# Performance work log

Hardware: AMD Instinct MI355X
Metric: run time of the kernel (lower is better)

Reference implementation:

```python
import jax, jax.numpy as jnp
import numpy as np

SHIFT = 1  # module's random shift_direction, fixed to +1 for determinism
B, C, H, W_SP = 1024, 512, 7, 7


def setup_inputs() -> dict:
    key = jax.random.key(0)
    k1, k2 = jax.random.split(key)
    x = jax.random.normal(k1, (B, C, H, W_SP), dtype=jnp.float32)
    W = jax.random.normal(k2, (256, 3, 3, 512), dtype=jnp.float32)
    return {"x": x, "W": W}


def _forward(x, W):
    # unfold along H with kernel (3,1), padding (1,0):
    # patches[b,c,kh,h,w] = x_padded[b,c,h+kh,w]
    xp = jnp.pad(x, ((0, 0), (0, 0), (1, 1), (0, 0)))
    t2 = jnp.stack([xp[:, :, k:k + H, :] for k in range(3)], axis=2)  # (B,512,3,7,7)
    # split channels 512 -> (2,256), move group dim next to H
    t2 = t2.reshape(B, 2, 256, 3, H, W_SP)
    t2 = t2.transpose(0, 2, 3, 4, 1, 5)          # (B,256,3,7,2,7)
    t2 = t2.reshape(B, 256, 3, 14, W_SP)         # interleave (h,group) -> 14
    t2 = jnp.roll(t2, SHIFT, axis=3)             # shift along interleaved dim
    t2 = t2.reshape(B, 256, 3, 7, 2, W_SP).sum(axis=4)  # (B,256,3,7,7)
    t2 = t2.transpose(0, 1, 3, 2, 4)             # (B,256,7,3,7) = (m,l,n,j,w)
    # second shift + unfold along w with kernel 3, padding 1
    t3 = jnp.roll(t2, SHIFT, axis=4)
    tp = jnp.pad(t3, ((0, 0), (0, 0), (0, 0), (0, 0), (1, 1)))
    t3u = jnp.stack([tp[..., k:k + W_SP] for k in range(3)], axis=4)  # (B,256,7,3,3,7) = (m,l,n,j,k,p)
    # torch einsum 'mlnjok, ljki -> mnoi' with o = output position, k = kernel tap
    out = jnp.einsum('mlnjkp,ljki->mpni', t3u, W)  # wait: check axis order below
    # Note: torch permutes (m,c,h,j,kernel,pos)->(m,c,h,j,pos,kernel) before einsum,
    # so contraction is over (l,j,kernel) and output is (m, n=h, o=pos, i).
    out = jnp.einsum('mlnjkp,ljki->mnpi', t3u, W)  # (B,7,7,512)
    return out.transpose(0, 3, 1, 2)              # (B,512,7,7)


def reference(x, W):
    return _forward(x, W)
```

## Files before the change

kernel.cpp:

```cpp
#include <hip/hip_runtime.h>
#include <hip/hip_bf16.h>


typedef __bf16 bf16x8 __attribute__((ext_vector_type(8)));
typedef float f32x4 __attribute__((ext_vector_type(4)));
typedef unsigned int u32;

#define VT_OFFSET (4u << 20)
#define VT_BYTES  (7168ull * 7 * 768 * 2)
#define WS_NEED   (VT_OFFSET + VT_BYTES)

__device__ __forceinline__ void gload_lds16(const void* g, void* l) {
    __builtin_amdgcn_global_load_lds(
        (const __attribute__((address_space(1))) u32*)g,
        (__attribute__((address_space(3))) u32*)l, 16, 0, 0);
}

__global__ __launch_bounds__(256) void prep_w(const float* __restrict__ Wg,
                                              __bf16* __restrict__ W2) {
    __shared__ float ws_[96][65];
    const int kt = blockIdx.x % 24;
    const int it_ = blockIdx.x / 24;
    const int K0 = kt * 96;
    const int I0 = it_ * 64;
    const int tid = threadIdx.x;

    #pragma unroll
    for (int t = 0; t < 6; ++t) {
        const int u = t * 256 + tid;
        const int row = u >> 4;
        const int f4 = u & 15;
        const float4 v = *(const float4*)(Wg + (size_t)(K0 + row) * 512 + I0 + f4 * 4);
        ws_[row][f4 * 4 + 0] = v.x;
        ws_[row][f4 * 4 + 1] = v.y;
        ws_[row][f4 * 4 + 2] = v.z;
        ws_[row][f4 * 4 + 3] = v.w;
    }
    __syncthreads();

    #pragma unroll
    for (int t = 0; t < 3; ++t) {
        const int u = t * 256 + tid;
        const int i = u / 12;
        const int rem = u - i * 12;
        const int tap = rem >> 2;
        const int q = rem & 3;
        bf16x8 o;
        #pragma unroll
        for (int e = 0; e < 8; ++e) {
            const int c_loc = q * 8 + e;
            o[e] = (__bf16)ws_[3 * c_loc + tap][i];
        }
        *(bf16x8*)(W2 + (size_t)(I0 + i) * 2304 + tap * 768 + 32 * kt + q * 8) = o;
    }
}

__global__ __launch_bounds__(256) void prep_v(const float* __restrict__ x,
                                              __bf16* __restrict__ Vt) {
    __shared__ float xs[256 * 49];
    const int b = blockIdx.x >> 1;
    const int g = blockIdx.x & 1;
    const int tid = threadIdx.x;

    {
        const float4* src0 = (const float4*)(x + ((size_t)b * 512 + g * 128) * 49);
        const float4* src1 = (const float4*)(x + ((size_t)b * 512 + 256 + g * 128) * 49);
        float4* dst0 = (float4*)xs;
        float4* dst1 = (float4*)(xs + 128 * 49);
        #pragma unroll
        for (int it = 0; it < 7; ++it) {
            const int q = it * 256 + tid;
            if (q < 1568) dst0[q] = src0[q];
        }
        #pragma unroll
        for (int it = 0; it < 7; ++it) {
            const int q = it * 256 + tid;
            if (q < 1568) dst1[q] = src1[q];
        }
    }
    __syncthreads();

    for (int h = 0; h < 7; ++h) {
        const int hm = (h + 6) % 7;
        for (int it = 0; it < 2; ++it) {
            const int u = it * 256 + tid;
            if (u < 336) {
                const int r = u / 48;
                const int k = u - r * 48;
                const int w = (r + 6) % 7;
                bf16x8 vv;
                #pragma unroll
                for (int e = 0; e < 8; ++e) {
                    const int c = k * 8 + e;
                    const int l = c / 3;
                    const int j = c - 3 * l;
                    const int r1 = h + j - 1;
                    const int r2 = hm + j - 1;
                    float v = 0.f;
                    if (r1 >= 0 && r1 < 7) v += xs[l * 49 + r1 * 7 + w];
                    if (r2 >= 0 && r2 < 7) v += xs[(128 + l) * 49 + r2 * 7 + w];
                    vv[e] = (__bf16)v;
                }
                *(bf16x8*)(Vt + (size_t)((b * 7 + h) * 7 + r) * 768 + g * 384 + k * 8) = vv;
            }
        }
    }
}

__global__ __launch_bounds__(256) void gemm_vt(const __bf16* __restrict__ Vt,
                                               const __bf16* __restrict__ W2,
                                               float* __restrict__ out) {
    __shared__ __align__(1024) char L[63616];

    const int tid = threadIdx.x;
    const int g0 = blockIdx.x;
    const int nb = (g0 >> 3) & 3;
    const int mb = ((g0 >> 5) << 3) | (g0 & 7);
    const int i0 = nb * 128;

    if (tid < 32) {
        const int off = (tid < 16) ? 7168 + tid * 4 : 14400 + (tid - 16) * 4;
        *(int*)(L + off) = 0;
    }

    int tsrc[2]; bool tok[2];
    #pragma unroll
    for (int it = 0; it < 2; ++it) {
        const int u = it * 256 + tid;
        tok[it] = (u < 448);
        const int bh = u / 28;
        const int rem = u - bh * 28;
        const int ct = rem >> 2;
        const int qs = rem & 3;
        const int q = qs ^ (ct & 3);
        tsrc[it] = ((mb * 16 + bh) * 7 + ct) * 1536 + q * 16;
    }
    int bsrc[6];
    #pragma unroll
    for (int it = 0; it < 6; ++it) {
        const int s = it * 256 + tid;
        const int tap = s >> 9;
        const int rem = s & 511;
        const int n = rem >> 2;
        const int qs = rem & 3;
        const int q = qs ^ ((n >> 1) & 3);
        bsrc[it] = ((i0 + n) * 2304 + tap * 768 + q * 8) * 2;
    }

    const int lane = tid & 63;
    const int wave = tid >> 6;
    const int wm = wave >> 1;
    const int wn = wave & 1;
    const int ln15 = lane & 15;
    const int gq = lane >> 4;

    int afoff[3][4], bfoff[3][4];
    #pragma unroll
    for (int tap = 0; tap < 3; ++tap) {
        #pragma unroll
        for (int mf = 0; mf < 4; ++mf) {
            const int bh_l = wm * 8 + mf * 2 + (ln15 >> 3);
            const int p = ln15 & 7;
            const int ct = p + tap - 1;
            afoff[tap][mf] = (ct >= 0 && ct <= 6)
                ? bh_l * 448 + ct * 64 + ((gq ^ (ct & 3)) * 16)
                : 7168;
        }
        #pragma unroll
        for (int nf = 0; nf < 4; ++nf) {
            const int n_l = wn * 64 + nf * 16 + ln15;
            bfoff[tap][nf] = tap * 8192 + n_l * 64 + ((gq ^ ((n_l >> 1) & 3)) * 16);
        }
    }

    f32x4 acc[4][4];
    #pragma unroll
    for (int a = 0; a < 4; ++a)
        #pragma unroll
        for (int bq = 0; bq < 4; ++bq) acc[a][bq] = (f32x4){0.f, 0.f, 0.f, 0.f};

    const char* VtB = (const char*)Vt;
    const char* W2B = (const char*)W2;

    auto stage = [&](int ck, int buf) {
        const char* vb = VtB + ck * 64;
        char* td = L + buf * 7232;
        if (tok[0]) gload_lds16(vb + tsrc[0], td + tid * 16);
        if (tok[1]) gload_lds16(vb + tsrc[1], td + 4096 + tid * 16);
        const char* wb = W2B + ck * 64;
        char* bd = L + 14464 + buf * 24576;
        #pragma unroll
        for (int it = 0; it < 6; ++it)
            gload_lds16(wb + bsrc[it], bd + it * 4096 + tid * 16);
    };

    stage(0, 0);
    __syncthreads();

    for (int chunk = 0; chunk < 24; ++chunk) {
        const int cur = chunk & 1;
        if (chunk < 23) stage(chunk + 1, cur ^ 1);

        const char* Tb = L + cur * 7232;
        const char* Bb = L + 14464 + cur * 24576;

        #pragma unroll
        for (int tap = 0; tap < 3; ++tap) {
            bf16x8 af[4], bfr[4];
            #pragma unroll
            for (int mf = 0; mf < 4; ++mf)
                af[mf] = *(const bf16x8*)(Tb + afoff[tap][mf]);
            #pragma unroll
            for (int nf = 0; nf < 4; ++nf)
                bfr[nf] = *(const bf16x8*)(Bb + bfoff[tap][nf]);
            #pragma unroll
            for (int mf = 0; mf < 4; ++mf)
                #pragma unroll
                for (int nf = 0; nf < 4; ++nf)
                    acc[mf][nf] = __builtin_amdgcn_mfma_f32_16x16x32_bf16(
                        af[mf], bfr[nf], acc[mf][nf], 0, 0, 0);
        }

        __syncthreads();
    }

    #pragma unroll
    for (int mf = 0; mf < 4; ++mf) {
        #pragma unroll
        for (int r = 0; r < 4; ++r) {
            const int mrow = gq * 4 + r;
            const int Mg_l = wm * 64 + mf * 16 + mrow;
            const int p = Mg_l & 7;
            if (p == 7) continue;
            const int bh_l = Mg_l >> 3;
            const int bhg = mb * 16 + bh_l;
            const int b = bhg / 7;
            const int h = bhg - 7 * b;
            #pragma unroll
            for (int nf = 0; nf < 4; ++nf) {
                const int i = i0 + wn * 64 + nf * 16 + ln15;
                out[(((size_t)b * 512 + i) * 7 + h) * 7 + p] = acc[mf][nf][r];
            }
        }
    }
}

__global__ __launch_bounds__(256) void gemm_shift(const float* __restrict__ x,
                                                  const __bf16* __restrict__ W2,
                                                  float* __restrict__ out) {
    __shared__ __bf16 T[16 * 10 * 40];
    __shared__ __bf16 Bt[128 * 104];

    const int tid = threadIdx.x;
    const int mb = blockIdx.x >> 2;
    const int nb = blockIdx.x & 3;
    const int i0 = nb * 128;

    const int cl  = tid & 31;
    const int bh0 = tid >> 5;
    const int bhg0 = mb * 16 + bh0;
    const int bhg1 = bhg0 + 8;
    const int b0 = bhg0 / 7, h0 = bhg0 - 7 * b0;
    const int b1 = bhg1 / 7, h1 = bhg1 - 7 * b1;
    const int hm0 = (h0 + 6) % 7, hm1 = (h1 + 6) % 7;

    for (int q = tid; q < 16 * 10 * 40 / 2; q += 256) ((int*)T)[q] = 0;

    const int lane = tid & 63;
    const int wave = tid >> 6;
    const int wm = wave >> 1;
    const int wn = wave & 1;
    const int ln15 = lane & 15;
    const int gq = lane >> 4;

    f32x4 acc[4][4];
    #pragma unroll
    for (int a = 0; a < 4; ++a)
        #pragma unroll
        for (int bq = 0; bq < 4; ++bq) acc[a][bq] = (f32x4){0.f, 0.f, 0.f, 0.f};

    __syncthreads();

    for (int chunk = 0; chunk < 24; ++chunk) {
        const int cg = chunk * 32 + cl;
        const int l = cg / 3;
        const int j = cg - 3 * l;
        {
            const int r1 = h0 + j - 1, r2 = hm0 + j - 1;
            float v[7] = {0.f, 0.f, 0.f, 0.f, 0.f, 0.f, 0.f};
            if (r1 >= 0 && r1 < 7) {
                const float* p1 = x + (((size_t)b0 * 512 + l) * 7 + r1) * 7;
                #pragma unroll
                for (int w = 0; w < 7; ++w) v[w] += p1[w];
            }
            if (r2 >= 0 && r2 < 7) {
                const float* p2 = x + (((size_t)b0 * 512 + 256 + l) * 7 + r2) * 7;
                #pragma unroll
                for (int w = 0; w < 7; ++w) v[w] += p2[w];
            }
            #pragma unroll
            for (int w = 0; w < 7; ++w)
                T[bh0 * 400 + ((w + 1) % 7 + 1) * 40 + cl] = (__bf16)v[w];
        }
        {
            const int r1 = h1 + j - 1, r2 = hm1 + j - 1;
            float v[7] = {0.f, 0.f, 0.f, 0.f, 0.f, 0.f, 0.f};
            if (r1 >= 0 && r1 < 7) {
                const float* p1 = x + (((size_t)b1 * 512 + l) * 7 + r1) * 7;
                #pragma unroll
                for (int w = 0; w < 7; ++w) v[w] += p1[w];
            }
            if (r2 >= 0 && r2 < 7) {
                const float* p2 = x + (((size_t)b1 * 512 + 256 + l) * 7 + r2) * 7;
                #pragma unroll
                for (int w = 0; w < 7; ++w) v[w] += p2[w];
            }
            #pragma unroll
            for (int w = 0; w < 7; ++w)
                T[(bh0 + 8) * 400 + ((w + 1) % 7 + 1) * 40 + cl] = (__bf16)v[w];
        }

        #pragma unroll
        for (int it = 0; it < 6; ++it) {
            const int u = it * 256 + tid;
            const int tap = u >> 9;
            const int rem = u & 511;
            const int n = rem >> 2;
            const int q = rem & 3;
            const float4 val = *(const float4*)(W2 + (size_t)(i0 + n) * 2304 +
                                                tap * 768 + chunk * 32 + q * 8);
            *(float4*)(&Bt[n * 104 + tap * 32 + q * 8]) = val;
        }

        __syncthreads();

        #pragma unroll
        for (int tap = 0; tap < 3; ++tap) {
            bf16x8 af[4], bfr[4];
            #pragma unroll
            for (int mf = 0; mf < 4; ++mf) {
                const int bh_l = wm * 8 + mf * 2 + (ln15 >> 3);
                const int p = ln15 & 7;
                af[mf] = *(const bf16x8*)(&T[(bh_l * 10 + p + tap) * 40 + gq * 8]);
            }
            #pragma unroll
            for (int nf = 0; nf < 4; ++nf) {
                const int n_l = wn * 64 + nf * 16 + ln15;
                bfr[nf] = *(const bf16x8*)(&Bt[n_l * 104 + tap * 32 + gq * 8]);
            }
            #pragma unroll
            for (int mf = 0; mf < 4; ++mf)
                #pragma unroll
                for (int nf = 0; nf < 4; ++nf)
                    acc[mf][nf] = __builtin_amdgcn_mfma_f32_16x16x32_bf16(
                        af[mf], bfr[nf], acc[mf][nf], 0, 0, 0);
        }

        __syncthreads();
    }

    #pragma unroll
    for (int mf = 0; mf < 4; ++mf) {
        #pragma unroll
        for (int r = 0; r < 4; ++r) {
            const int mrow = gq * 4 + r;
            const int Mg_l = wm * 64 + mf * 16 + mrow;
            const int p = Mg_l & 7;
            if (p == 7) continue;
            const int bh_l = Mg_l >> 3;
            const int bhg = mb * 16 + bh_l;
            const int b = bhg / 7;
            const int h = bhg - 7 * b;
            #pragma unroll
            for (int nf = 0; nf < 4; ++nf) {
                const int i = i0 + wn * 64 + nf * 16 + ln15;
                out[(((size_t)b * 512 + i) * 7 + h) * 7 + p] = acc[mf][nf][r];
            }
        }
    }
}

extern "C" void kernel_launch(void* const* d_in, const int* in_sizes, int n_in,
                              void* d_out, int out_size, void* d_ws, size_t ws_size,
                              hipStream_t stream) {
    const float* x  = (const float*)d_in[0];
    const float* Wg = (const float*)d_in[1];
    float* out = (float*)d_out;
    __bf16* W2 = (__bf16*)d_ws;

    prep_w<<<dim3(192), dim3(256), 0, stream>>>(Wg, W2);

    if (ws_size >= WS_NEED) {
        __bf16* Vt = (__bf16*)((char*)d_ws + VT_OFFSET);
        prep_v<<<dim3(2048), dim3(256), 0, stream>>>(x, Vt);
        gemm_vt<<<dim3(448 * 4), dim3(256), 0, stream>>>(Vt, W2, out);
    } else {
        gemm_shift<<<dim3(448 * 4), dim3(256), 0, stream>>>(x, W2, out);
    }
}
```

Measured before the change: 358.4 us.

## Deepen GEMM prefetch to two chunks with vmcnt-based waits and register-staged fragments

The GEMM main loop changes from single-chunk prefetch with __syncthreads to issuing loads two chunks ahead. Each thread now issues a uniform number of global-to-LDS loads, with idle threads sending theirs to a dummy LDS region, so that fixed vmcnt counts can be used for waiting. All fragments for a chunk are read from LDS into registers before a barrier. The buffer is then refilled while the MFMAs run. This aims to hide global memory latency better, at the cost of more registers for fragments and a small extra LDS area.

Result: no change. 360.5 us (+0.6%).

```diff
diff --git a/kernel.cpp b/kernel.cpp
--- a/kernel.cpp
+++ b/kernel.cpp
@@ -110,7 +110,7 @@
 __global__ __launch_bounds__(256) void gemm_vt(const __bf16* __restrict__ Vt,
                                                const __bf16* __restrict__ W2,
                                                float* __restrict__ out) {
-    __shared__ __align__(1024) char L[63616];
+    __shared__ __align__(1024) char L[64640];
 
     const int tid = threadIdx.x;
     const int g0 = blockIdx.x;
@@ -123,17 +123,20 @@
         *(int*)(L + off) = 0;
     }
 
-    int tsrc[2]; bool tok[2];
+    int tsrc[2];
     #pragma unroll
     for (int it = 0; it < 2; ++it) {
         const int u = it * 256 + tid;
-        tok[it] = (u < 448);
-        const int bh = u / 28;
-        const int rem = u - bh * 28;
-        const int ct = rem >> 2;
-        const int qs = rem & 3;
-        const int q = qs ^ (ct & 3);
-        tsrc[it] = ((mb * 16 + bh) * 7 + ct) * 1536 + q * 16;
+        if (u < 448) {
+            const int bh = u / 28;
+            const int rem = u - bh * 28;
+            const int ct = rem >> 2;
+            const int qs = rem & 3;
+            const int q = qs ^ (ct & 3);
+            tsrc[it] = ((mb * 16 + bh) * 7 + ct) * 1536 + q * 16;
+        } else {
+            tsrc[it] = 0;
+        }
     }
     int bsrc[6];
     #pragma unroll
@@ -185,8 +188,11 @@
     auto stage = [&](int ck, int buf) {
         const char* vb = VtB + ck * 64;
         char* td = L + buf * 7232;
-        if (tok[0]) gload_lds16(vb + tsrc[0], td + tid * 16);
-        if (tok[1]) gload_lds16(vb + tsrc[1], td + 4096 + tid * 16);
+        gload_lds16(vb + tsrc[0], td + tid * 16);
+        if (tid < 192)
+            gload_lds16(vb + tsrc[1], td + 4096 + tid * 16);
+        else
+            gload_lds16(VtB, L + 63616 + (tid - 192) * 16);
         const char* wb = W2B + ck * 64;
         char* bd = L + 14464 + buf * 24576;
         #pragma unroll
@@ -195,33 +201,43 @@
     };
 
     stage(0, 0);
-    __syncthreads();
+    stage(1, 1);
+    asm volatile("s_waitcnt lgkmcnt(0)" ::: "memory");
 
     for (int chunk = 0; chunk < 24; ++chunk) {
         const int cur = chunk & 1;
-        if (chunk < 23) stage(chunk + 1, cur ^ 1);
+
+        if (chunk < 23) asm volatile("s_waitcnt vmcnt(8)" ::: "memory");
+        else            asm volatile("s_waitcnt vmcnt(0)" ::: "memory");
+        __builtin_amdgcn_s_barrier();
 
         const char* Tb = L + cur * 7232;
         const char* Bb = L + 14464 + cur * 24576;
 
+        bf16x8 af[3][4], bfr[3][4];
         #pragma unroll
         for (int tap = 0; tap < 3; ++tap) {
-            bf16x8 af[4], bfr[4];
             #pragma unroll
             for (int mf = 0; mf < 4; ++mf)
-                af[mf] = *(const bf16x8*)(Tb + afoff[tap][mf]);
+                af[tap][mf] = *(const bf16x8*)(Tb + afoff[tap][mf]);
             #pragma unroll
             for (int nf = 0; nf < 4; ++nf)
-                bfr[nf] = *(const bf16x8*)(Bb + bfoff[tap][nf]);
+                bfr[tap][nf] = *(const bf16x8*)(Bb + bfoff[tap][nf]);
+        }
+        asm volatile("s_waitcnt lgkmcnt(0)" ::: "memory");
+        __builtin_amdgcn_sched_barrier(0);
+        __builtin_amdgcn_s_barrier();
+
+        if (chunk + 2 < 24) stage(chunk + 2, cur);
+
+        #pragma unroll
+        for (int tap = 0; tap < 3; ++tap)
             #pragma unroll
             for (int mf = 0; mf < 4; ++mf)
                 #pragma unroll
                 for (int nf = 0; nf < 4; ++nf)
                     acc[mf][nf] = __builtin_amdgcn_mfma_f32_16x16x32_bf16(
-                        af[mf], bfr[nf], acc[mf][nf], 0, 0, 0);
-        }
-
-        __syncthreads();
+                        af[tap][mf], bfr[tap][nf], acc[mf][nf], 0, 0, 0);
     }
 
     #pragma unroll
```

## Pre-swizzle weights into MFMA fragment order and load B directly from global

Applied to the files above, without the earlier changes.

Adds a prep kernel that writes the bf16 weights in the exact per-lane fragment layout used by the MFMA B operand. The GEMM then reads B fragments straight from global/L2 into registers instead of staging them through LDS, which cuts LDS use from about 62KB to 14KB so two blocks can fit per CU. The cost is that B loads are no longer prefetched asynchronously and their latency sits on the path of every chunk, along with more global read traffic per block.

New measurement: 367.7 us. 1.03x slower.

```diff
diff --git a/kernel.cpp b/kernel.cpp
--- a/kernel.cpp
+++ b/kernel.cpp
@@ -16,8 +16,8 @@
         (__attribute__((address_space(3))) u32*)l, 16, 0, 0);
 }
 
-__global__ __launch_bounds__(256) void prep_w(const float* __restrict__ Wg,
-                                              __bf16* __restrict__ W2) {
+__global__ __launch_bounds__(256) void prep_wf(const float* __restrict__ Wg,
+                                               __bf16* __restrict__ W2f) {
     __shared__ float ws_[96][65];
     const int kt = blockIdx.x % 24;
     const int it_ = blockIdx.x / 24;
@@ -41,16 +41,56 @@
     #pragma unroll
     for (int t = 0; t < 3; ++t) {
         const int u = t * 256 + tid;
+        const int q = u / 192;
+        const int tap = (u / 64) % 3;
+        const int i_loc = u & 63;
+        bf16x8 o;
+        #pragma unroll
+        for (int e = 0; e < 8; ++e)
+            o[e] = (__bf16)ws_[3 * (q * 8 + e) + tap][i_loc];
+        const int i_g = I0 + i_loc;
+        const int nb = i_g >> 7;
+        const int r = i_g & 127;
+        const int wnf = r >> 4;
+        const int l15 = r & 15;
+        const int unit = (((nb * 24 + kt) * 3 + tap) * 8 + wnf) * 64 + q * 16 + l15;
+        *(bf16x8*)(W2f + (size_t)unit * 8) = o;
+    }
+}
+
+__global__ __launch_bounds__(256) void prep_w(const float* __restrict__ Wg,
+                                              __bf16* __restrict__ W2) {
+    __shared__ float ws_[96][65];
+    const int kt = blockIdx.x % 24;
+    const int it_ = blockIdx.x / 24;
+    const int K0 = kt * 96;
+    const int I0 = it_ * 64;
+    const int tid = threadIdx.x;
+
+    #pragma unroll
+    for (int t = 0; t < 6; ++t) {
+        const int u = t * 256 + tid;
+        const int row = u >> 4;
+        const int f4 = u & 15;
+        const float4 v = *(const float4*)(Wg + (size_t)(K0 + row) * 512 + I0 + f4 * 4);
+        ws_[row][f4 * 4 + 0] = v.x;
+        ws_[row][f4 * 4 + 1] = v.y;
+        ws_[row][f4 * 4 + 2] = v.z;
+        ws_[row][f4 * 4 + 3] = v.w;
+    }
+    __syncthreads();
+
+    #pragma unroll
+    for (int t = 0; t < 3; ++t) {
+        const int u = t * 256 + tid;
         const int i = u / 12;
         const int rem = u - i * 12;
         const int tap = rem >> 2;
         const int q = rem & 3;
         bf16x8 o;
         #pragma unroll
-        for (int e = 0; e < 8; ++e) {
-            const int c_loc = q * 8 + e;
-            o[e] = (__bf16)ws_[3 * c_loc + tap][i];
-        }
+        for (int e = 0; e < 8; ++e)
+            o[e] = (__bf16)ws_[3 * (q * 8 + e) + tap][i];
         *(bf16x8*)(W2 + (size_t)(I0 + i) * 2304 + tap * 768 + 32 * kt + q * 8) = o;
     }
 }
@@ -107,16 +147,15 @@
     }
 }
 
-__global__ __launch_bounds__(256) void gemm_vt(const __bf16* __restrict__ Vt,
-                                               const __bf16* __restrict__ W2,
-                                               float* __restrict__ out) {
-    __shared__ __align__(1024) char L[63616];
+__global__ __launch_bounds__(256, 2) void gemm_vt(const __bf16* __restrict__ Vt,
+                                                  const __bf16* __restrict__ W2f,
+                                                  float* __restrict__ out) {
+    __shared__ __align__(1024) char L[14464];
 
     const int tid = threadIdx.x;
     const int g0 = blockIdx.x;
     const int nb = (g0 >> 3) & 3;
     const int mb = ((g0 >> 5) << 3) | (g0 & 7);
-    const int i0 = nb * 128;
 
     if (tid < 32) {
         const int off = (tid < 16) ? 7168 + tid * 4 : 14400 + (tid - 16) * 4;
@@ -135,17 +174,6 @@
         const int q = qs ^ (ct & 3);
         tsrc[it] = ((mb * 16 + bh) * 7 + ct) * 1536 + q * 16;
     }
-    int bsrc[6];
-    #pragma unroll
-    for (int it = 0; it < 6; ++it) {
-        const int s = it * 256 + tid;
-        const int tap = s >> 9;
-        const int rem = s & 511;
-        const int n = rem >> 2;
-        const int qs = rem & 3;
-        const int q = qs ^ ((n >> 1) & 3);
-        bsrc[it] = ((i0 + n) * 2304 + tap * 768 + q * 8) * 2;
-    }
 
     const int lane = tid & 63;
     const int wave = tid >> 6;
@@ -154,7 +182,12 @@
     const int ln15 = lane & 15;
     const int gq = lane >> 4;
 
-    int afoff[3][4], bfoff[3][4];
+    int boff[4];
+    #pragma unroll
+    for (int nf = 0; nf < 4; ++nf)
+        boff[nf] = nb * 589824 + (wn * 4 + nf) * 1024 + lane * 16;
+
+    int afoff[3][4];
     #pragma unroll
     for (int tap = 0; tap < 3; ++tap) {
         #pragma unroll
@@ -166,11 +199,6 @@
                 ? bh_l * 448 + ct * 64 + ((gq ^ (ct & 3)) * 16)
                 : 7168;
         }
-        #pragma unroll
-        for (int nf = 0; nf < 4; ++nf) {
-            const int n_l = wn * 64 + nf * 16 + ln15;
-            bfoff[tap][nf] = tap * 8192 + n_l * 64 + ((gq ^ ((n_l >> 1) & 3)) * 16);
-        }
     }
 
     f32x4 acc[4][4];
@@ -180,45 +208,45 @@
         for (int bq = 0; bq < 4; ++bq) acc[a][bq] = (f32x4){0.f, 0.f, 0.f, 0.f};
 
     const char* VtB = (const char*)Vt;
-    const char* W2B = (const char*)W2;
-
-    auto stage = [&](int ck, int buf) {
-        const char* vb = VtB + ck * 64;
-        char* td = L + buf * 7232;
-        if (tok[0]) gload_lds16(vb + tsrc[0], td + tid * 16);
-        if (tok[1]) gload_lds16(vb + tsrc[1], td + 4096 + tid * 16);
-        const char* wb = W2B + ck * 64;
-        char* bd = L + 14464 + buf * 24576;
-        #pragma unroll
-        for (int it = 0; it < 6; ++it)
-            gload_lds16(wb + bsrc[it], bd + it * 4096 + tid * 16);
-    };
-
-    stage(0, 0);
+    const char* W2fB = (const char*)W2f;
+
+    {
+        const char* vb = VtB;
+        if (tok[0]) gload_lds16(vb + tsrc[0], L + tid * 16);
+        if (tok[1]) gload_lds16(vb + tsrc[1], L + 4096 + tid * 16);
+    }
     __syncthreads();
 
     for (int chunk = 0; chunk < 24; ++chunk) {
         const int cur = chunk & 1;
-        if (chunk < 23) stage(chunk + 1, cur ^ 1);
+        if (chunk < 23) {
+            const char* vb = VtB + (chunk + 1) * 64;
+            char* td = L + (cur ^ 1) * 7232;
+            if (tok[0]) gload_lds16(vb + tsrc[0], td + tid * 16);
+            if (tok[1]) gload_lds16(vb + tsrc[1], td + 4096 + tid * 16);
+        }
+
+        const char* wb = W2fB + chunk * 24576;
+        bf16x8 bfr[3][4];
+        #pragma unroll
+        for (int tap = 0; tap < 3; ++tap)
+            #pragma unroll
+            for (int nf = 0; nf < 4; ++nf)
+                bfr[tap][nf] = *(const bf16x8*)(wb + tap * 8192 + boff[nf]);
 
         const char* Tb = L + cur * 7232;
-        const char* Bb = L + 14464 + cur * 24576;
-
         #pragma unroll
         for (int tap = 0; tap < 3; ++tap) {
-            bf16x8 af[4], bfr[4];
+            bf16x8 af[4];
             #pragma unroll
             for (int mf = 0; mf < 4; ++mf)
                 af[mf] = *(const bf16x8*)(Tb + afoff[tap][mf]);
             #pragma unroll
-            for (int nf = 0; nf < 4; ++nf)
-                bfr[nf] = *(const bf16x8*)(Bb + bfoff[tap][nf]);
-            #pragma unroll
             for (int mf = 0; mf < 4; ++mf)
                 #pragma unroll
                 for (int nf = 0; nf < 4; ++nf)
                     acc[mf][nf] = __builtin_amdgcn_mfma_f32_16x16x32_bf16(
-                        af[mf], bfr[nf], acc[mf][nf], 0, 0, 0);
+                        af[mf], bfr[tap][nf], acc[mf][nf], 0, 0, 0);
         }
 
         __syncthreads();
@@ -238,7 +266,7 @@
             const int h = bhg - 7 * b;
             #pragma unroll
             for (int nf = 0; nf < 4; ++nf) {
-                const int i = i0 + wn * 64 + nf * 16 + ln15;
+                const int i = nb * 128 + wn * 64 + nf * 16 + ln15;
                 out[(((size_t)b * 512 + i) * 7 + h) * 7 + p] = acc[mf][nf][r];
             }
         }
@@ -386,15 +414,16 @@
     const float* x  = (const float*)d_in[0];
     const float* Wg = (const float*)d_in[1];
     float* out = (float*)d_out;
-    __bf16* W2 = (__bf16*)d_ws;
-
-    prep_w<<<dim3(192), dim3(256), 0, stream>>>(Wg, W2);
 
     if (ws_size >= WS_NEED) {
+        __bf16* W2f = (__bf16*)d_ws;
         __bf16* Vt = (__bf16*)((char*)d_ws + VT_OFFSET);
+        prep_wf<<<dim3(192), dim3(256), 0, stream>>>(Wg, W2f);
         prep_v<<<dim3(2048), dim3(256), 0, stream>>>(x, Vt);
-        gemm_vt<<<dim3(448 * 4), dim3(256), 0, stream>>>(Vt, W2, out);
+        gemm_vt<<<dim3(448 * 4), dim3(256), 0, stream>>>(Vt, W2f, out);
     } else {
+        __bf16* W2 = (__bf16*)d_ws;
+        prep_w<<<dim3(192), dim3(256), 0, stream>>>(Wg, W2);
         gemm_shift<<<dim3(448 * 4), dim3(256), 0, stream>>>(x, W2, out);
     }
 }
```
